# Performance work log

Hardware: AMD Instinct MI355X
Metric: run time of the kernel (lower is better)

## Reference

```python
import jax, jax.numpy as jnp
import numpy as np

N, E, D, EDIM, L, H = 50000, 800000, 128, 16, 3, 8


def setup_inputs() -> dict:
    key = jax.random.key(0)
    ks = jax.random.split(key, 16)
    inner = (L + 1) * D  # concat of input + 3 GCN layer outputs
    return {
        "x": jax.random.normal(ks[0], (N, D), jnp.float32),
        "edge_index": jax.random.randint(ks[1], (2, E), 0, N),
        "edge_attr": jax.random.normal(ks[2], (E, EDIM), jnp.float32),
        "dag_edge_index": jax.random.randint(ks[3], (2, E), 0, N),
        "W_v": jax.random.normal(ks[4], (D, D), jnp.float32) * 0.05,
        "W_qk": jax.random.normal(ks[5], (D, 2 * D), jnp.float32) * 0.05,
        "gcn_W": jax.random.normal(ks[6], (L, D, D), jnp.float32) * 0.05,
        "gcn_b": jnp.zeros((L, D), jnp.float32),
        "gcn_root": jax.random.normal(ks[7], (L, D), jnp.float32) * 0.05,
        "gcn_We": jax.random.normal(ks[8], (L, EDIM, D), jnp.float32) * 0.05,
        "gcn_be": jnp.zeros((L, D), jnp.float32),
        "bn_gamma": jnp.ones((inner,), jnp.float32),
        "bn_beta": jnp.zeros((inner,), jnp.float32),
        "W_se": jax.random.normal(ks[9], (inner, D), jnp.float32) * 0.05,
        "b_se": jnp.zeros((D,), jnp.float32),
        "W_out": jax.random.normal(ks[10], (D, D), jnp.float32) * 0.05,
        "b_out": jnp.zeros((D,), jnp.float32),
    }


def reference(x, edge_index, edge_attr, dag_edge_index, W_v, W_qk, gcn_W, gcn_b,
              gcn_root, gcn_We, gcn_be, bn_gamma, bn_beta, W_se, b_se, W_out, b_out):
    n = x.shape[0]
    row, col = edge_index[0], edge_index[1]  # source j, target i

    def gcn_layer(h, Wl, bl, root, We, be):
        h = h @ Wl + bl                                   # [N, D]
        e = edge_attr @ We + be                           # [E, D]
        deg = jax.ops.segment_sum(jnp.ones(row.shape[0], h.dtype), row, num_segments=n) + 1.0
        dis = deg ** -0.5
        norm = dis[row] * dis[col]                        # [E]
        msg = norm[:, None] * jax.nn.relu(h[row] + e)     # gather + per-edge transform
        agg = jax.ops.segment_sum(msg, col, num_segments=n)  # scatter-add at target
        return agg + jax.nn.relu(h + root) / deg[:, None]

    # StructureExtractor: 3 GCN layers, concat skip features
    xs = [x]
    h = x
    for i in range(gcn_W.shape[0]):
        h = jax.nn.relu(gcn_layer(h, gcn_W[i], gcn_b[i], gcn_root[i], gcn_We[i], gcn_be[i]))
        xs.append(h)
    xc = jnp.concatenate(xs, axis=-1)                     # [N, 4D]
    mu = xc.mean(0)
    var = xc.var(0)
    xc = (xc - mu) / jnp.sqrt(var + 1e-5) * bn_gamma + bn_beta  # BatchNorm1d (batch stats)
    x_struct = xc @ W_se + b_se                           # [N, D]

    # sparse multi-head attention over dag_rr_edge_index
    v = x @ W_v
    qk = x_struct @ W_qk
    d = x.shape[1]
    qk_src_tbl, qk_dst_tbl = qk[:, :d], qk[:, d:]         # chunk(2): (qk_j, qk_i)
    hd = d // H
    scale = hd ** -0.5
    src, dst = dag_edge_index[0], dag_edge_index[1]
    qj = qk_src_tbl[src].reshape(-1, H, hd)
    qi = qk_dst_tbl[dst].reshape(-1, H, hd)
    logits = (qi * qj).sum(-1) * scale                    # [E, H]
    m = jax.ops.segment_max(logits, dst, num_segments=n)
    p = jnp.exp(logits - m[dst])
    s = jax.ops.segment_sum(p, dst, num_segments=n)
    attn = p / s[dst]                                     # per-destination softmax
    vj = v[src].reshape(-1, H, hd)
    out = jax.ops.segment_sum(vj * attn[..., None], dst, num_segments=n).reshape(-1, d)
    return out @ W_out + b_out
```

## Files before the change

kernel.cpp:

```cpp
#include <hip/hip_runtime.h>

#define D 128
#define EDIMC 16
#define GCAP 64

typedef __attribute__((ext_vector_type(8))) short short8v;
typedef __attribute__((ext_vector_type(4))) float f32x4;
typedef __attribute__((ext_vector_type(2))) float f32x2;
typedef __attribute__((ext_vector_type(2))) _Float16 h16x2;

__device__ __forceinline__ float asf(unsigned u){ union{unsigned u; float f;} v; v.u = u; return v.f; }
__device__ __forceinline__ unsigned asu(float f){ union{float f; unsigned u;} v; v.f = f; return v.u; }
__device__ __forceinline__ unsigned short f2bf(float f){
    unsigned u = asu(f);
    unsigned r = (u + 0x7fffu + ((u >> 16) & 1u)) >> 16;
    return (unsigned short)r;
}
__device__ __forceinline__ unsigned packbf(float lo, float hi){
    return (unsigned)f2bf(lo) | ((unsigned)f2bf(hi) << 16);
}
__device__ __forceinline__ unsigned packh(float a, float b){
    union{ h16x2 h; unsigned u; } v;
    v.h = (h16x2){(_Float16)a, (_Float16)b};
    return v.u;
}
__device__ __forceinline__ h16x2 ash2(unsigned u){ union{unsigned u; h16x2 h;} v; v.u = u; return v.h; }

__global__ void scatter_all(const int* __restrict__ row, const int* __restrict__ col,
                            const int* __restrict__ asrc_in, const int* __restrict__ adst,
                            int E, const float* __restrict__ eattr,
                            int* __restrict__ cr, int* __restrict__ curg, int* __restrict__ curd,
                            int* __restrict__ gsrcS, uint4* __restrict__ epermS,
                            int* __restrict__ asrcS)
{
    int e = blockIdx.x*blockDim.x + threadIdx.x;
    if(e >= E) return;
    int r = row[e], c = col[e];
    atomicAdd(&cr[r], 1);
    int pg = atomicAdd(&curg[c], 1);
    if(pg < GCAP){
        int slot = c*GCAP + pg;
        gsrcS[slot] = r;
        const float4* s4 = (const float4*)(eattr + (size_t)e*EDIMC);
        float4 a = s4[0], b = s4[1], cc2 = s4[2], d = s4[3];
        uint4 o0, o1;
        o0.x = packh(a.x, a.y);    o0.y = packh(a.z, a.w);
        o0.z = packh(b.x, b.y);    o0.w = packh(b.z, b.w);
        o1.x = packh(cc2.x, cc2.y);o1.y = packh(cc2.z, cc2.w);
        o1.z = packh(d.x, d.y);    o1.w = packh(d.z, d.w);
        epermS[(size_t)slot*2 + 0] = o0;
        epermS[(size_t)slot*2 + 1] = o1;
    }
    int s2 = asrc_in[e], d2 = adst[e];
    int pd = atomicAdd(&curd[d2], 1);
    if(pd < GCAP) asrcS[d2*GCAP + pd] = s2;
}

__global__ void deg_fin2(const int* __restrict__ cr, float* __restrict__ deg,
                         float* __restrict__ dis, int N){
    int i = blockIdx.x*blockDim.x + threadIdx.x;
    if(i < N){ float d = (float)cr[i] + 1.0f; deg[i] = d; dis[i] = rsqrtf(d); }
}

__global__ void prep_weights(const float* __restrict__ gW, const float* __restrict__ Wv,
                             const float* __restrict__ Wqk, const float* __restrict__ Wout,
                             const float* __restrict__ gWe,
                             unsigned short* __restrict__ gWt, unsigned short* __restrict__ Wvt,
                             unsigned short* __restrict__ Wqkt, unsigned short* __restrict__ Woutt,
                             unsigned* __restrict__ wpk)
{
    int b = blockIdx.x, j = threadIdx.x;
    if(b < 384){
        int l = b >> 7, k = b & 127;
        if(j < 128) gWt[(size_t)l*16384 + (size_t)j*128 + k] = f2bf(gW[(size_t)l*16384 + (size_t)k*128 + j]);
    } else if(b < 512){
        int k = b - 384;
        if(j < 128) Wvt[(size_t)j*128 + k] = f2bf(Wv[(size_t)k*128 + j]);
    } else if(b < 640){
        int k = b - 512;
        Wqkt[(size_t)j*128 + k] = f2bf(Wqk[(size_t)k*256 + j]);
    } else if(b < 768){
        int k = b - 640;
        if(j < 128) Woutt[(size_t)j*128 + k] = f2bf(Wout[(size_t)k*128 + j]);
    } else {
        int t = b - 768; int l = t >> 3, kk = t & 7;
        if(j < 128){
            const float* W = gWe + (size_t)l*EDIMC*D;
            wpk[(size_t)l*1024 + kk*128 + j] = packh(W[(size_t)(2*kk)*D + j], W[(size_t)(2*kk+1)*D + j]);
        }
    }
}

__global__ void prep_x(const float* __restrict__ x, unsigned* __restrict__ xbf,
                       unsigned* __restrict__ xc, int N){
    int idx = blockIdx.x*blockDim.x + threadIdx.x;
    if(idx >= N*64) return;
    int i = idx >> 6, c2 = idx & 63;
    float a = x[(size_t)i*128 + c2*2], b = x[(size_t)i*128 + c2*2 + 1];
    unsigned p = packbf(a, b);
    xbf[idx] = p;
    xc[(size_t)i*256 + c2] = p;
}

template<int OUT>
__global__ __launch_bounds__(256) void gemm_mfma(
    const unsigned short* __restrict__ A, const unsigned short* __restrict__ Bt,
    const float* __restrict__ bias, void* __restrict__ Cout,
    int M, int K, int Nc)
{
    int tid = threadIdx.x;
    int wid = tid >> 6, lane = tid & 63;
    int bm = blockIdx.y*64 + wid*16;
    int bn = blockIdx.x*64;
    int lr = lane & 15;
    int kg = lane >> 4;
    int arow = bm + lr; if(arow >= M) arow = M - 1;
    f32x4 acc[4];
    #pragma unroll
    for(int i = 0; i < 4; i++) acc[i] = (f32x4){0.f,0.f,0.f,0.f};
    for(int k0 = 0; k0 < K; k0 += 32){
        short8v a = *(const short8v*)(A + (size_t)arow*K + k0 + kg*8);
        #pragma unroll
        for(int nf = 0; nf < 4; nf++){
            short8v b = *(const short8v*)(Bt + (size_t)(bn + nf*16 + lr)*K + k0 + kg*8);
            acc[nf] = __builtin_amdgcn_mfma_f32_16x16x32_bf16(a, b, acc[nf], 0, 0, 0);
        }
    }
    int crow = bm + kg*4;
    #pragma unroll
    for(int nf = 0; nf < 4; nf++){
        int col = bn + nf*16 + lr;
        float bs = bias ? bias[col] : 0.f;
        #pragma unroll
        for(int r = 0; r < 4; r++){
            int rw = crow + r;
            if(rw < M){
                float val = acc[nf][r] + bs;
                if(OUT == 1)
                    ((unsigned short*)Cout)[(size_t)rw*Nc + col] = f2bf(val);
                else if(OUT == 2)
                    ((_Float16*)Cout)[(size_t)rw*Nc + col] = (_Float16)val;
                else
                    ((float*)Cout)[(size_t)rw*Nc + col] = val;
            }
        }
    }
}

__device__ __forceinline__ void edge_acc5(
    uint4 ea0, uint4 ea1, unsigned hu, float nm,
    const unsigned* __restrict__ w0, const unsigned* __restrict__ w1,
    float be0, float be1, float& a0, float& a1)
{
    float ev0 = be0, ev1 = be1;
    unsigned ea[8] = {ea0.x, ea0.y, ea0.z, ea0.w, ea1.x, ea1.y, ea1.z, ea1.w};
    #pragma unroll
    for(int kk = 0; kk < 8; kk++){
        ev0 = __builtin_amdgcn_fdot2(ash2(ea[kk]), ash2(w0[kk]), ev0, false);
        ev1 = __builtin_amdgcn_fdot2(ash2(ea[kk]), ash2(w1[kk]), ev1, false);
    }
    float sx = fmaxf(asf(hu << 16) + ev0, 0.f);
    float sy = fmaxf(asf(hu & 0xffff0000u) + ev1, 0.f);
    a0 += nm*sx; a1 += nm*sy;
}

__global__ __launch_bounds__(256) void gcn_gather_v6(
    const unsigned* __restrict__ hlin,
    const int* __restrict__ curg,
    const int* __restrict__ gsrcS,
    const uint4* __restrict__ epermS,
    const float* __restrict__ dis,
    const unsigned* __restrict__ wpk_l,
    const float* __restrict__ be,
    const float* __restrict__ root, const float* __restrict__ deg,
    unsigned* __restrict__ xc, unsigned* __restrict__ hcur, int blk, int N)
{
    int lane = threadIdx.x & 63;
    int node = __builtin_amdgcn_readfirstlane((int)((blockIdx.x*blockDim.x + threadIdx.x) >> 6));
    if(node >= N) return;
    unsigned w0[8], w1[8];
    const uint2* wp2 = (const uint2*)wpk_l;
    #pragma unroll
    for(int kk = 0; kk < 8; kk++){
        uint2 t = wp2[(size_t)kk*64 + lane];
        w0[kk] = t.x; w1[kk] = t.y;
    }
    f32x2 be2 = ((const f32x2*)be)[lane];
    f32x2 rt2 = ((const f32x2*)root)[lane];
    float disn = dis[node];
    int s0 = node*GCAP;
    int s1 = s0 + min(curg[node], GCAP);
    float a0 = 0.f, a1 = 0.f;
    int s = s0;
    for(; s + 4 <= s1; s += 4){
        int r0 = gsrcS[s+0], r1 = gsrcS[s+1], r2 = gsrcS[s+2], r3 = gsrcS[s+3];
        float d0 = dis[r0], d1 = dis[r1], d2 = dis[r2], d3 = dis[r3];
        unsigned h0 = hlin[(size_t)r0*64 + lane];
        unsigned h1 = hlin[(size_t)r1*64 + lane];
        unsigned h2 = hlin[(size_t)r2*64 + lane];
        unsigned h3 = hlin[(size_t)r3*64 + lane];
        uint4 e00 = epermS[(size_t)(s+0)*2+0], e01 = epermS[(size_t)(s+0)*2+1];
        uint4 e10 = epermS[(size_t)(s+1)*2+0], e11 = epermS[(size_t)(s+1)*2+1];
        uint4 e20 = epermS[(size_t)(s+2)*2+0], e21 = epermS[(size_t)(s+2)*2+1];
        uint4 e30 = epermS[(size_t)(s+3)*2+0], e31 = epermS[(size_t)(s+3)*2+1];
        edge_acc5(e00, e01, h0, d0*disn, w0, w1, be2.x, be2.y, a0, a1);
        edge_acc5(e10, e11, h1, d1*disn, w0, w1, be2.x, be2.y, a0, a1);
        edge_acc5(e20, e21, h2, d2*disn, w0, w1, be2.x, be2.y, a0, a1);
        edge_acc5(e30, e31, h3, d3*disn, w0, w1, be2.x, be2.y, a0, a1);
    }
    for(; s < s1; s++){
        int r0 = gsrcS[s];
        float d0 = dis[r0];
        unsigned h0 = hlin[(size_t)r0*64 + lane];
        uint4 e00 = epermS[(size_t)s*2+0], e01 = epermS[(size_t)s*2+1];
        edge_acc5(e00, e01, h0, d0*disn, w0, w1, be2.x, be2.y, a0, a1);
    }
    unsigned hlu = hlin[(size_t)node*64 + lane];
    float hlx = asf(hlu << 16), hly = asf(hlu & 0xffff0000u);
    float dinv = 1.f/deg[node];
    float v0 = fmaxf(a0 + fmaxf(hlx + rt2.x, 0.f)*dinv, 0.f);
    float v1 = fmaxf(a1 + fmaxf(hly + rt2.y, 0.f)*dinv, 0.f);
    unsigned p = packbf(v0, v1);
    hcur[(size_t)node*64 + lane] = p;
    xc[(size_t)node*256 + (size_t)blk*64 + lane] = p;
}

__global__ __launch_bounds__(256) void bn_stats_bf(
    const unsigned* __restrict__ xc, int N, float* __restrict__ stats)
{
    int c0 = threadIdx.x;
    int rows_per = (N + gridDim.x - 1)/gridDim.x;
    int r0 = blockIdx.x*rows_per, r1 = min(N, r0 + rows_per);
    float s0=0, q0=0, s1=0, q1=0;
    for(int r = r0; r < r1; r++){
        unsigned u = xc[(size_t)r*256 + c0];
        float a = asf(u << 16), b = asf(u & 0xffff0000u);
        s0 += a; q0 += a*a; s1 += b; q1 += b*b;
    }
    atomicAdd(&stats[2*c0+0], s0);  atomicAdd(&stats[512 + 2*c0+0], q0);
    atomicAdd(&stats[2*c0+1], s1);  atomicAdd(&stats[512 + 2*c0+1], q1);
}

__global__ void fold_wse_t(const float* __restrict__ Wse, const float* __restrict__ gamma,
                           const float* __restrict__ stats, float Ninv,
                           unsigned short* __restrict__ Wse2t)
{
    int k = blockIdx.x, j = threadIdx.x;
    float mu  = stats[k]*Ninv;
    float var = stats[512+k]*Ninv - mu*mu;
    float sc  = gamma[k]*rsqrtf(var + 1e-5f);
    Wse2t[(size_t)j*512 + k] = f2bf(Wse[(size_t)k*128 + j]*sc);
}
__global__ void fold_bse(const float* __restrict__ Wse, const float* __restrict__ gamma,
                         const float* __restrict__ beta, const float* __restrict__ bse,
                         const float* __restrict__ stats, float Ninv, float* __restrict__ bse2)
{
    int j = threadIdx.x;
    float acc = bse[j];
    for(int k = 0; k < 512; k++){
        float mu  = stats[k]*Ninv;
        float var = stats[512+k]*Ninv - mu*mu;
        float sc  = gamma[k]*rsqrtf(var + 1e-5f);
        float sh  = beta[k] - mu*sc;
        acc += sh*Wse[(size_t)k*128 + j];
    }
    bse2[j] = acc;
}

__global__ __launch_bounds__(256) void attn_fused_v6(
    const unsigned* __restrict__ qk,
    const unsigned* __restrict__ v,
    const int* __restrict__ curd, const int* __restrict__ asrcS,
    unsigned* __restrict__ out, int N)
{
    int lane = threadIdx.x & 63;
    int node = __builtin_amdgcn_readfirstlane((int)((blockIdx.x*blockDim.x + threadIdx.x) >> 6));
    if(node >= N) return;
    int cnt = min(curd[node], GCAP);
    int s0 = node*GCAP, s1 = s0 + cnt;
    float o0 = 0.f, o1 = 0.f;
    if(cnt > 0){
        h16x2 qi2 = ash2(qk[(size_t)node*128 + 64 + lane]);
        float m = -INFINITY, ssum = 0.f, a0 = 0.f, a1 = 0.f;
        int s = s0;
        for(; s + 4 <= s1; s += 4){
            int sr0 = asrcS[s+0], sr1 = asrcS[s+1], sr2 = asrcS[s+2], sr3 = asrcS[s+3];
            unsigned qj[4], vv[4];
            qj[0] = qk[(size_t)sr0*128 + lane];  vv[0] = v[(size_t)sr0*64 + lane];
            qj[1] = qk[(size_t)sr1*128 + lane];  vv[1] = v[(size_t)sr1*64 + lane];
            qj[2] = qk[(size_t)sr2*128 + lane];  vv[2] = v[(size_t)sr2*64 + lane];
            qj[3] = qk[(size_t)sr3*128 + lane];  vv[3] = v[(size_t)sr3*64 + lane];
            float l[4];
            #pragma unroll
            for(int j = 0; j < 4; j++){
                float p = __builtin_amdgcn_fdot2(qi2, ash2(qj[j]), 0.f, false);
                p += __shfl_xor(p, 1);
                p += __shfl_xor(p, 2);
                p += __shfl_xor(p, 4);
                l[j] = p*0.25f;
            }
            #pragma unroll
            for(int j = 0; j < 4; j++){
                float mn = fmaxf(m, l[j]);
                float sc = __expf(m - mn);
                float p  = __expf(l[j] - mn);
                h16x2 v2 = ash2(vv[j]);
                ssum = ssum*sc + p;
                a0 = a0*sc + p*(float)v2.x;
                a1 = a1*sc + p*(float)v2.y;
                m = mn;
            }
        }
        for(; s < s1; s++){
            int srx = asrcS[s];
            h16x2 qj2 = ash2(qk[(size_t)srx*128 + lane]);
            h16x2 v2  = ash2(v [(size_t)srx*64  + lane]);
            float p = __builtin_amdgcn_fdot2(qi2, qj2, 0.f, false);
            p += __shfl_xor(p, 1);
            p += __shfl_xor(p, 2);
            p += __shfl_xor(p, 4);
            float l = p*0.25f;
            float mn = fmaxf(m, l);
            float sc = __expf(m - mn);
            float pe = __expf(l - mn);
            ssum = ssum*sc + pe;
            a0 = a0*sc + pe*(float)v2.x;
            a1 = a1*sc + pe*(float)v2.y;
            m = mn;
        }
        float inv = 1.f/ssum;
        o0 = a0*inv; o1 = a1*inv;
    }
    out[(size_t)node*64 + lane] = packbf(o0, o1);
}

extern "C" void kernel_launch(void* const* d_in, const int* in_sizes, int n_in,
                              void* d_out, int out_size, void* d_ws, size_t ws_size,
                              hipStream_t stream)
{
    const float* x     = (const float*)d_in[0];
    const int*   ei    = (const int*)  d_in[1];
    const float* eattr = (const float*)d_in[2];
    const int*   dei   = (const int*)  d_in[3];
    const float* Wv    = (const float*)d_in[4];
    const float* Wqk   = (const float*)d_in[5];
    const float* gW    = (const float*)d_in[6];
    const float* gb    = (const float*)d_in[7];
    const float* groot = (const float*)d_in[8];
    const float* gWe   = (const float*)d_in[9];
    const float* gbe   = (const float*)d_in[10];
    const float* gamma = (const float*)d_in[11];
    const float* beta  = (const float*)d_in[12];
    const float* Wse   = (const float*)d_in[13];
    const float* bse   = (const float*)d_in[14];
    const float* Wout  = (const float*)d_in[15];
    const float* bout  = (const float*)d_in[16];

    const int N = in_sizes[0]/D;
    const int E = in_sizes[1]/2;
    const int L = in_sizes[7]/D;

    float* ws = (float*)d_ws;
    size_t o = 0;
    auto alloc = [&](size_t n){ size_t r = o; o += (n + 63) & ~(size_t)63; return r; };
    size_t f_deg   = alloc((size_t)N);
    size_t f_dis   = alloc((size_t)N);
    size_t f_hlin  = alloc((size_t)N*64);
    size_t f_hcur  = alloc((size_t)N*64);
    size_t f_xbf   = alloc((size_t)N*64);
    size_t f_xc    = alloc((size_t)N*256);
    size_t f_st    = alloc(1024);
    size_t f_b2    = alloc(128);
    size_t f_cnt   = alloc((size_t)N*3);
    size_t f_gsrc  = alloc((size_t)N*GCAP);
    size_t f_asrc  = alloc((size_t)N*GCAP);
    size_t f_wgt   = alloc(90112 + 64);
    size_t f_wpk   = alloc(3*1024);
    size_t f_ep    = alloc((size_t)N*GCAP*8);
    (void)ws_size;

    float* deg  = ws + f_deg;   float* dis  = ws + f_dis;
    unsigned* hlin = (unsigned*)(ws + f_hlin);
    unsigned* hcur = (unsigned*)(ws + f_hcur);
    unsigned* xbf  = (unsigned*)(ws + f_xbf);
    unsigned* xc   = (unsigned*)(ws + f_xc);
    float* stats = ws + f_st;   float* bse2 = ws + f_b2;
    int* cnts = (int*)(ws + f_cnt);
    int* cr = cnts, *curg = cnts + N, *curd = cnts + 2*N;
    int* gsrcS = (int*)(ws + f_gsrc);
    int* asrcS = (int*)(ws + f_asrc);
    unsigned short* wbase = (unsigned short*)(ws + f_wgt);
    unsigned short* gWt   = wbase;
    unsigned short* Wvt   = gWt + 3*128*128;
    unsigned short* Wqkt  = Wvt + 128*128;
    unsigned short* Woutt = Wqkt + 256*128;
    unsigned short* Wse2t = Woutt + 128*128;
    unsigned* wpk = (unsigned*)(ws + f_wpk);
    uint4* epermS = (uint4*)(ws + f_ep);
    unsigned* qk   = (unsigned*)(ws + f_ep);
    unsigned* vbuf = qk   + (size_t)N*128;
    unsigned* xst  = vbuf + (size_t)N*64;
    unsigned* aout = xst  + (size_t)N*64;

    const int* e_row = ei;        const int* e_col = ei + E;
    const int* a_src = dei;       const int* a_dst = dei + E;

    dim3 blk256(256);
    int gE = (E+255)/256, gN = (N+255)/256;
    int gNode = ((size_t)N*64 + 255)/256;
    int gMy = (N+63)/64;

    hipMemsetAsync(cnts, 0, (size_t)N*3*sizeof(int), stream);
    scatter_all<<<gE, blk256, 0, stream>>>(e_row, e_col, a_src, a_dst, E, eattr,
                                           cr, curg, curd, gsrcS, epermS, asrcS);
    deg_fin2<<<gN, blk256, 0, stream>>>(cr, deg, dis, N);

    prep_weights<<<768 + 8*L, blk256, 0, stream>>>(gW, Wv, Wqk, Wout, gWe,
                                                   gWt, Wvt, Wqkt, Woutt, wpk);
    prep_x<<<gNode, blk256, 0, stream>>>(x, xbf, xc, N);

    const unsigned* hin = xbf;
    for(int l = 0; l < L; l++){
        dim3 g(2, gMy);
        gemm_mfma<1><<<g, blk256, 0, stream>>>((const unsigned short*)hin, gWt + (size_t)l*D*D,
                                               gb + (size_t)l*D, hlin, N, 128, 128);
        gcn_gather_v6<<<gNode, blk256, 0, stream>>>(hlin, curg, gsrcS, epermS, dis,
                                                    wpk + (size_t)l*1024, gbe + (size_t)l*D,
                                                    groot + (size_t)l*D, deg, xc, hcur, l+1, N);
        hin = hcur;
    }

    hipMemsetAsync(stats, 0, 1024*sizeof(float), stream);
    bn_stats_bf<<<256, blk256, 0, stream>>>(xc, N, stats);
    float Ninv = 1.0f/(float)N;
    fold_wse_t<<<512, 128, 0, stream>>>(Wse, gamma, stats, Ninv, Wse2t);
    fold_bse<<<1, 128, 0, stream>>>(Wse, gamma, beta, bse, stats, Ninv, bse2);

    {   dim3 g(2, gMy);
        gemm_mfma<1><<<g, blk256, 0, stream>>>((const unsigned short*)xc, Wse2t, bse2, xst, N, 512, 128);
    }
    {   dim3 g(2, gMy);
        gemm_mfma<2><<<g, blk256, 0, stream>>>((const unsigned short*)xbf, Wvt, nullptr, vbuf, N, 128, 128);
    }
    {   dim3 g(4, gMy);
        gemm_mfma<2><<<g, blk256, 0, stream>>>((const unsigned short*)xst, Wqkt, nullptr, qk, N, 128, 256);
    }

    attn_fused_v6<<<gNode, blk256, 0, stream>>>(qk, vbuf, curd, asrcS, aout, N);

    {   dim3 g(2, gMy);
        gemm_mfma<0><<<g, blk256, 0, stream>>>((const unsigned short*)aout, Woutt, bout, (float*)d_out, N, 128, 128);
    }
}
```

Before: 698.3 us.

## Merge prep kernels and index edge attributes by edge id instead of slot

Fuses the edge scatter, x conversion and weight prep kernels into one launch, and also merges the two BN-fold kernels. Edge attributes are now converted to fp16 in edge order (E*8 words) instead of being scattered into a per-slot buffer of N*GCAP*8 words. The gather stores (src, edge id) pairs and reads attributes indirectly. This shrinks the scattered write traffic and the number of launches. In exchange, the gather kernel does non-contiguous attribute reads, and separate workspace buffers replace the aliased ones.

After: 696.1 us. No clear change (-0.3%).

```diff
diff --git a/kernel.cpp b/kernel.cpp
--- a/kernel.cpp
+++ b/kernel.cpp
@@ -26,80 +26,76 @@
 }
 __device__ __forceinline__ h16x2 ash2(unsigned u){ union{unsigned u; h16x2 h;} v; v.u = u; return v.h; }
 
-__global__ void scatter_all(const int* __restrict__ row, const int* __restrict__ col,
-                            const int* __restrict__ asrc_in, const int* __restrict__ adst,
-                            int E, const float* __restrict__ eattr,
-                            int* __restrict__ cr, int* __restrict__ curg, int* __restrict__ curd,
-                            int* __restrict__ gsrcS, uint4* __restrict__ epermS,
-                            int* __restrict__ asrcS)
-{
-    int e = blockIdx.x*blockDim.x + threadIdx.x;
-    if(e >= E) return;
-    int r = row[e], c = col[e];
-    atomicAdd(&cr[r], 1);
-    int pg = atomicAdd(&curg[c], 1);
-    if(pg < GCAP){
-        int slot = c*GCAP + pg;
-        gsrcS[slot] = r;
+__global__ __launch_bounds__(256) void prep_all(
+    const int* __restrict__ row, const int* __restrict__ col,
+    const int* __restrict__ asrc_in, const int* __restrict__ adst,
+    int E, int N, int gE, int gX, int L,
+    const float* __restrict__ eattr, const float* __restrict__ x,
+    const float* __restrict__ gW, const float* __restrict__ Wv,
+    const float* __restrict__ Wqk, const float* __restrict__ Wout,
+    const float* __restrict__ gWe,
+    int* __restrict__ cr, int* __restrict__ curg, int* __restrict__ curd,
+    int2* __restrict__ gslot, int* __restrict__ asrcS, unsigned* __restrict__ eattrh,
+    unsigned* __restrict__ xbf, unsigned* __restrict__ xc,
+    unsigned short* __restrict__ gWt, unsigned short* __restrict__ Wvt,
+    unsigned short* __restrict__ Wqkt, unsigned short* __restrict__ Woutt,
+    unsigned* __restrict__ wpk)
+{
+    int b = blockIdx.x, tid = threadIdx.x;
+    if(b < gE){
+        int e = b*256 + tid;
+        if(e >= E) return;
         const float4* s4 = (const float4*)(eattr + (size_t)e*EDIMC);
-        float4 a = s4[0], b = s4[1], cc2 = s4[2], d = s4[3];
-        uint4 o0, o1;
-        o0.x = packh(a.x, a.y);    o0.y = packh(a.z, a.w);
-        o0.z = packh(b.x, b.y);    o0.w = packh(b.z, b.w);
-        o1.x = packh(cc2.x, cc2.y);o1.y = packh(cc2.z, cc2.w);
-        o1.z = packh(d.x, d.y);    o1.w = packh(d.z, d.w);
-        epermS[(size_t)slot*2 + 0] = o0;
-        epermS[(size_t)slot*2 + 1] = o1;
-    }
-    int s2 = asrc_in[e], d2 = adst[e];
-    int pd = atomicAdd(&curd[d2], 1);
-    if(pd < GCAP) asrcS[d2*GCAP + pd] = s2;
+        float4 a = s4[0], bb = s4[1], cc2 = s4[2], d = s4[3];
+        unsigned* dst8 = eattrh + (size_t)e*8;
+        dst8[0] = packh(a.x, a.y);    dst8[1] = packh(a.z, a.w);
+        dst8[2] = packh(bb.x, bb.y);  dst8[3] = packh(bb.z, bb.w);
+        dst8[4] = packh(cc2.x, cc2.y);dst8[5] = packh(cc2.z, cc2.w);
+        dst8[6] = packh(d.x, d.y);    dst8[7] = packh(d.z, d.w);
+        int r = row[e], c = col[e];
+        atomicAdd(&cr[r], 1);
+        int pg = atomicAdd(&curg[c], 1);
+        if(pg < GCAP) gslot[c*GCAP + pg] = make_int2(r, e);
+        int s2 = asrc_in[e], d2 = adst[e];
+        int pd = atomicAdd(&curd[d2], 1);
+        if(pd < GCAP) asrcS[d2*GCAP + pd] = s2;
+    } else if(b < gE + gX){
+        int idx = (b - gE)*256 + tid;
+        if(idx >= N*64) return;
+        int i = idx >> 6, c2 = idx & 63;
+        float a = x[(size_t)i*128 + c2*2], bb = x[(size_t)i*128 + c2*2 + 1];
+        unsigned p = packbf(a, bb);
+        xbf[idx] = p;
+        xc[(size_t)i*256 + c2] = p;
+    } else {
+        int wb = b - gE - gX;
+        int j = tid;
+        if(wb < 384){
+            int l = wb >> 7, k = wb & 127;
+            if(j < 128) gWt[(size_t)l*16384 + (size_t)j*128 + k] = f2bf(gW[(size_t)l*16384 + (size_t)k*128 + j]);
+        } else if(wb < 512){
+            int k = wb - 384;
+            if(j < 128) Wvt[(size_t)j*128 + k] = f2bf(Wv[(size_t)k*128 + j]);
+        } else if(wb < 640){
+            int k = wb - 512;
+            Wqkt[(size_t)j*128 + k] = f2bf(Wqk[(size_t)k*256 + j]);
+        } else if(wb < 768){
+            int k = wb - 640;
+            if(j < 128) Woutt[(size_t)j*128 + k] = f2bf(Wout[(size_t)k*128 + j]);
+        } else {
+            int t = wb - 768; int l = t >> 3, kk = t & 7;
+            if(j < 128){
+                const float* W = gWe + (size_t)l*EDIMC*D;
+                wpk[(size_t)l*1024 + kk*128 + j] = packh(W[(size_t)(2*kk)*D + j], W[(size_t)(2*kk+1)*D + j]);
+            }
+        }
+    }
 }
 
 __global__ void deg_fin2(const int* __restrict__ cr, float* __restrict__ deg,
                          float* __restrict__ dis, int N){
     int i = blockIdx.x*blockDim.x + threadIdx.x;
     if(i < N){ float d = (float)cr[i] + 1.0f; deg[i] = d; dis[i] = rsqrtf(d); }
-}
-
-__global__ void prep_weights(const float* __restrict__ gW, const float* __restrict__ Wv,
-                             const float* __restrict__ Wqk, const float* __restrict__ Wout,
-                             const float* __restrict__ gWe,
-                             unsigned short* __restrict__ gWt, unsigned short* __restrict__ Wvt,
-                             unsigned short* __restrict__ Wqkt, unsigned short* __restrict__ Woutt,
-                             unsigned* __restrict__ wpk)
-{
-    int b = blockIdx.x, j = threadIdx.x;
-    if(b < 384){
-        int l = b >> 7, k = b & 127;
-        if(j < 128) gWt[(size_t)l*16384 + (size_t)j*128 + k] = f2bf(gW[(size_t)l*16384 + (size_t)k*128 + j]);
-    } else if(b < 512){
-        int k = b - 384;
-        if(j < 128) Wvt[(size_t)j*128 + k] = f2bf(Wv[(size_t)k*128 + j]);
-    } else if(b < 640){
-        int k = b - 512;
-        Wqkt[(size_t)j*128 + k] = f2bf(Wqk[(size_t)k*256 + j]);
-    } else if(b < 768){
-        int k = b - 640;
-        if(j < 128) Woutt[(size_t)j*128 + k] = f2bf(Wout[(size_t)k*128 + j]);
-    } else {
-        int t = b - 768; int l = t >> 3, kk = t & 7;
-        if(j < 128){
-            const float* W = gWe + (size_t)l*EDIMC*D;
-            wpk[(size_t)l*1024 + kk*128 + j] = packh(W[(size_t)(2*kk)*D + j], W[(size_t)(2*kk+1)*D + j]);
-        }
-    }
-}
-
-__global__ void prep_x(const float* __restrict__ x, unsigned* __restrict__ xbf,
-                       unsigned* __restrict__ xc, int N){
-    int idx = blockIdx.x*blockDim.x + threadIdx.x;
-    if(idx >= N*64) return;
-    int i = idx >> 6, c2 = idx & 63;
-    float a = x[(size_t)i*128 + c2*2], b = x[(size_t)i*128 + c2*2 + 1];
-    unsigned p = packbf(a, b);
-    xbf[idx] = p;
-    xc[(size_t)i*256 + c2] = p;
 }
 
 template<int OUT>
@@ -164,11 +160,11 @@
     a0 += nm*sx; a1 += nm*sy;
 }
 
-__global__ __launch_bounds__(256) void gcn_gather_v6(
+__global__ __launch_bounds__(256) void gcn_gather_v7(
     const unsigned* __restrict__ hlin,
     const int* __restrict__ curg,
-    const int* __restrict__ gsrcS,
-    const uint4* __restrict__ epermS,
+    const int2* __restrict__ gslot,
+    const unsigned* __restrict__ eattrh,
     const float* __restrict__ dis,
     const unsigned* __restrict__ wpk_l,
     const float* __restrict__ be,
@@ -193,26 +189,31 @@
     float a0 = 0.f, a1 = 0.f;
     int s = s0;
     for(; s + 4 <= s1; s += 4){
-        int r0 = gsrcS[s+0], r1 = gsrcS[s+1], r2 = gsrcS[s+2], r3 = gsrcS[s+3];
-        float d0 = dis[r0], d1 = dis[r1], d2 = dis[r2], d3 = dis[r3];
-        unsigned h0 = hlin[(size_t)r0*64 + lane];
-        unsigned h1 = hlin[(size_t)r1*64 + lane];
-        unsigned h2 = hlin[(size_t)r2*64 + lane];
-        unsigned h3 = hlin[(size_t)r3*64 + lane];
-        uint4 e00 = epermS[(size_t)(s+0)*2+0], e01 = epermS[(size_t)(s+0)*2+1];
-        uint4 e10 = epermS[(size_t)(s+1)*2+0], e11 = epermS[(size_t)(s+1)*2+1];
-        uint4 e20 = epermS[(size_t)(s+2)*2+0], e21 = epermS[(size_t)(s+2)*2+1];
-        uint4 e30 = epermS[(size_t)(s+3)*2+0], e31 = epermS[(size_t)(s+3)*2+1];
+        int2 sl0 = gslot[s+0], sl1 = gslot[s+1], sl2 = gslot[s+2], sl3 = gslot[s+3];
+        float d0 = dis[sl0.x], d1 = dis[sl1.x], d2 = dis[sl2.x], d3 = dis[sl3.x];
+        unsigned h0 = hlin[(size_t)sl0.x*64 + lane];
+        unsigned h1 = hlin[(size_t)sl1.x*64 + lane];
+        unsigned h2 = hlin[(size_t)sl2.x*64 + lane];
+        unsigned h3 = hlin[(size_t)sl3.x*64 + lane];
+        uint4 e00 = *(const uint4*)(eattrh + (size_t)sl0.y*8);
+        uint4 e01 = *(const uint4*)(eattrh + (size_t)sl0.y*8 + 4);
+        uint4 e10 = *(const uint4*)(eattrh + (size_t)sl1.y*8);
+        uint4 e11 = *(const uint4*)(eattrh + (size_t)sl1.y*8 + 4);
+        uint4 e20 = *(const uint4*)(eattrh + (size_t)sl2.y*8);
+        uint4 e21 = *(const uint4*)(eattrh + (size_t)sl2.y*8 + 4);
+        uint4 e30 = *(const uint4*)(eattrh + (size_t)sl3.y*8);
+        uint4 e31 = *(const uint4*)(eattrh + (size_t)sl3.y*8 + 4);
         edge_acc5(e00, e01, h0, d0*disn, w0, w1, be2.x, be2.y, a0, a1);
         edge_acc5(e10, e11, h1, d1*disn, w0, w1, be2.x, be2.y, a0, a1);
         edge_acc5(e20, e21, h2, d2*disn, w0, w1, be2.x, be2.y, a0, a1);
         edge_acc5(e30, e31, h3, d3*disn, w0, w1, be2.x, be2.y, a0, a1);
     }
     for(; s < s1; s++){
-        int r0 = gsrcS[s];
-        float d0 = dis[r0];
-        unsigned h0 = hlin[(size_t)r0*64 + lane];
-        uint4 e00 = epermS[(size_t)s*2+0], e01 = epermS[(size_t)s*2+1];
+        int2 sl0 = gslot[s];
+        float d0 = dis[sl0.x];
+        unsigned h0 = hlin[(size_t)sl0.x*64 + lane];
+        uint4 e00 = *(const uint4*)(eattrh + (size_t)sl0.y*8);
+        uint4 e01 = *(const uint4*)(eattrh + (size_t)sl0.y*8 + 4);
         edge_acc5(e00, e01, h0, d0*disn, w0, w1, be2.x, be2.y, a0, a1);
     }
     unsigned hlu = hlin[(size_t)node*64 + lane];
@@ -241,33 +242,31 @@
     atomicAdd(&stats[2*c0+1], s1);  atomicAdd(&stats[512 + 2*c0+1], q1);
 }
 
-__global__ void fold_wse_t(const float* __restrict__ Wse, const float* __restrict__ gamma,
-                           const float* __restrict__ stats, float Ninv,
-                           unsigned short* __restrict__ Wse2t)
-{
-    int k = blockIdx.x, j = threadIdx.x;
-    float mu  = stats[k]*Ninv;
-    float var = stats[512+k]*Ninv - mu*mu;
-    float sc  = gamma[k]*rsqrtf(var + 1e-5f);
-    Wse2t[(size_t)j*512 + k] = f2bf(Wse[(size_t)k*128 + j]*sc);
-}
-__global__ void fold_bse(const float* __restrict__ Wse, const float* __restrict__ gamma,
+__global__ void fold_all(const float* __restrict__ Wse, const float* __restrict__ gamma,
                          const float* __restrict__ beta, const float* __restrict__ bse,
-                         const float* __restrict__ stats, float Ninv, float* __restrict__ bse2)
-{
-    int j = threadIdx.x;
-    float acc = bse[j];
-    for(int k = 0; k < 512; k++){
-        float mu  = stats[k]*Ninv;
-        float var = stats[512+k]*Ninv - mu*mu;
-        float sc  = gamma[k]*rsqrtf(var + 1e-5f);
-        float sh  = beta[k] - mu*sc;
-        acc += sh*Wse[(size_t)k*128 + j];
-    }
-    bse2[j] = acc;
-}
-
-__global__ __launch_bounds__(256) void attn_fused_v6(
+                         const float* __restrict__ stats, float Ninv,
+                         unsigned short* __restrict__ Wse2t, float* __restrict__ bse2)
+{
+    int b = blockIdx.x, j = threadIdx.x;
+    if(b < 512){
+        float mu  = stats[b]*Ninv;
+        float var = stats[512+b]*Ninv - mu*mu;
+        float sc  = gamma[b]*rsqrtf(var + 1e-5f);
+        Wse2t[(size_t)j*512 + b] = f2bf(Wse[(size_t)b*128 + j]*sc);
+    } else {
+        float acc = bse[j];
+        for(int k = 0; k < 512; k++){
+            float mu  = stats[k]*Ninv;
+            float var = stats[512+k]*Ninv - mu*mu;
+            float sc  = gamma[k]*rsqrtf(var + 1e-5f);
+            float sh  = beta[k] - mu*sc;
+            acc += sh*Wse[(size_t)k*128 + j];
+        }
+        bse2[j] = acc;
+    }
+}
+
+__global__ __launch_bounds__(256) void attn_fused_v7(
     const unsigned* __restrict__ qk,
     const unsigned* __restrict__ v,
     const int* __restrict__ curd, const int* __restrict__ asrcS,
@@ -372,11 +371,15 @@
     size_t f_st    = alloc(1024);
     size_t f_b2    = alloc(128);
     size_t f_cnt   = alloc((size_t)N*3);
-    size_t f_gsrc  = alloc((size_t)N*GCAP);
+    size_t f_gslot = alloc((size_t)N*GCAP*2);
     size_t f_asrc  = alloc((size_t)N*GCAP);
+    size_t f_eah   = alloc((size_t)E*8);
     size_t f_wgt   = alloc(90112 + 64);
     size_t f_wpk   = alloc(3*1024);
-    size_t f_ep    = alloc((size_t)N*GCAP*8);
+    size_t f_qk    = alloc((size_t)N*128);
+    size_t f_vb    = alloc((size_t)N*64);
+    size_t f_xst   = alloc((size_t)N*64);
+    size_t f_aout  = alloc((size_t)N*64);
     (void)ws_size;
 
     float* deg  = ws + f_deg;   float* dis  = ws + f_dis;
@@ -387,8 +390,9 @@
     float* stats = ws + f_st;   float* bse2 = ws + f_b2;
     int* cnts = (int*)(ws + f_cnt);
     int* cr = cnts, *curg = cnts + N, *curd = cnts + 2*N;
-    int* gsrcS = (int*)(ws + f_gsrc);
+    int2* gslot = (int2*)(ws + f_gslot);
     int* asrcS = (int*)(ws + f_asrc);
+    unsigned* eattrh = (unsigned*)(ws + f_eah);
     unsigned short* wbase = (unsigned short*)(ws + f_wgt);
     unsigned short* gWt   = wbase;
     unsigned short* Wvt   = gWt + 3*128*128;
@@ -396,11 +400,10 @@
     unsigned short* Woutt = Wqkt + 256*128;
     unsigned short* Wse2t = Woutt + 128*128;
     unsigned* wpk = (unsigned*)(ws + f_wpk);
-    uint4* epermS = (uint4*)(ws + f_ep);
-    unsigned* qk   = (unsigned*)(ws + f_ep);
-    unsigned* vbuf = qk   + (size_t)N*128;
-    unsigned* xst  = vbuf + (size_t)N*64;
-    unsigned* aout = xst  + (size_t)N*64;
+    unsigned* qk   = (unsigned*)(ws + f_qk);
+    unsigned* vbuf = (unsigned*)(ws + f_vb);
+    unsigned* xst  = (unsigned*)(ws + f_xst);
+    unsigned* aout = (unsigned*)(ws + f_aout);
 
     const int* e_row = ei;        const int* e_col = ei + E;
     const int* a_src = dei;       const int* a_dst = dei + E;
@@ -408,23 +411,23 @@
     dim3 blk256(256);
     int gE = (E+255)/256, gN = (N+255)/256;
     int gNode = ((size_t)N*64 + 255)/256;
+    int gX = gNode;
     int gMy = (N+63)/64;
 
     hipMemsetAsync(cnts, 0, (size_t)N*3*sizeof(int), stream);
-    scatter_all<<<gE, blk256, 0, stream>>>(e_row, e_col, a_src, a_dst, E, eattr,
-                                           cr, curg, curd, gsrcS, epermS, asrcS);
+    prep_all<<<gE + gX + 768 + 8*L, blk256, 0, stream>>>(
+        e_row, e_col, a_src, a_dst, E, N, gE, gX, L,
+        eattr, x, gW, Wv, Wqk, Wout, gWe,
+        cr, curg, curd, gslot, asrcS, eattrh,
+        xbf, xc, gWt, Wvt, Wqkt, Woutt, wpk);
     deg_fin2<<<gN, blk256, 0, stream>>>(cr, deg, dis, N);
-
-    prep_weights<<<768 + 8*L, blk256, 0, stream>>>(gW, Wv, Wqk, Wout, gWe,
-                                                   gWt, Wvt, Wqkt, Woutt, wpk);
-    prep_x<<<gNode, blk256, 0, stream>>>(x, xbf, xc, N);
 
     const unsigned* hin = xbf;
     for(int l = 0; l < L; l++){
         dim3 g(2, gMy);
         gemm_mfma<1><<<g, blk256, 0, stream>>>((const unsigned short*)hin, gWt + (size_t)l*D*D,
                                                gb + (size_t)l*D, hlin, N, 128, 128);
-        gcn_gather_v6<<<gNode, blk256, 0, stream>>>(hlin, curg, gsrcS, epermS, dis,
+        gcn_gather_v7<<<gNode, blk256, 0, stream>>>(hlin, curg, gslot, eattrh, dis,
                                                     wpk + (size_t)l*1024, gbe + (size_t)l*D,
                                                     groot + (size_t)l*D, deg, xc, hcur, l+1, N);
         hin = hcur;
@@ -433,8 +436,7 @@
     hipMemsetAsync(stats, 0, 1024*sizeof(float), stream);
     bn_stats_bf<<<256, blk256, 0, stream>>>(xc, N, stats);
     float Ninv = 1.0f/(float)N;
-    fold_wse_t<<<512, 128, 0, stream>>>(Wse, gamma, stats, Ninv, Wse2t);
-    fold_bse<<<1, 128, 0, stream>>>(Wse, gamma, beta, bse, stats, Ninv, bse2);
+    fold_all<<<513, 128, 0, stream>>>(Wse, gamma, beta, bse, stats, Ninv, Wse2t, bse2);
 
     {   dim3 g(2, gMy);
         gemm_mfma<1><<<g, blk256, 0, stream>>>((const unsigned short*)xc, Wse2t, bse2, xst, N, 512, 128);
@@ -446,7 +448,7 @@
         gemm_mfma<2><<<g, blk256, 0, stream>>>((const unsigned short*)xst, Wqkt, nullptr, qk, N, 128, 256);
     }
 
-    attn_fused_v6<<<gNode, blk256, 0, stream>>>(qk, vbuf, curd, asrcS, aout, N);
+    attn_fused_v7<<<gNode, blk256, 0, stream>>>(qk, vbuf, curd, asrcS, aout, N);
 
     {   dim3 g(2, gMy);
         gemm_mfma<0><<<g, blk256, 0, stream>>>((const unsigned short*)aout, Woutt, bout, (float*)d_out, N, 128, 128);
```
